# Optimization experiments

Measured on AMD Instinct MI355X. Metric: run time of the kernel, lower is better.

Reference implementation:

```python
import jax, jax.numpy as jnp
import numpy as np

B, T, D, E, K, OUT = 512, 2048, 32, 64, 8, 1024  # batch, tokens, feat(=32 hardcoded), experts, top-k, expert out dim


def setup_inputs() -> dict:
    key = jax.random.key(0)
    k0, k1, k2, k3 = jax.random.split(key, 4)
    x = jax.random.normal(k0, (B, T, D), jnp.float32)
    gate_w = jax.random.normal(k1, (E, D), jnp.float32) / np.sqrt(D)
    gate_b = jnp.zeros((E,), jnp.float32)
    # stacked expert Linear(32*k -> OUT): weight [E, OUT, D*K], bias [E, OUT]
    expert_w = jax.random.normal(k2, (E, OUT, D * K), jnp.float32) / np.sqrt(D * K)
    expert_b = jnp.zeros((E, OUT), jnp.float32)
    # gumbel noise for multinomial-without-replacement sampling (Gumbel top-k trick)
    gumbel = jax.random.gumbel(k3, (B, E, T), jnp.float32)
    return {"x": x, "gate_w": gate_w, "gate_b": gate_b,
            "expert_w": expert_w, "expert_b": expert_b, "gumbel": gumbel}


def reference(x, gate_w, gate_b, expert_w, expert_b, gumbel):
    # gate logits [B,T,E]; softmax over TOKEN axis (dim=-2 in torch)
    logits = jnp.einsum('btd,ed->bte', x, gate_w) + gate_b
    logp = jax.nn.log_softmax(logits, axis=-2)          # [B,T,E]
    # g = probs transposed to [B,E,T]; multinomial(k, no replacement) == top-k of log p + Gumbel
    scores = jnp.transpose(logp, (0, 2, 1)) + gumbel    # [B,E,T]
    _, idx = jax.lax.top_k(scores, K)                   # [B,E,K] sampled token indices
    # gather k tokens per (batch, expert): [B,E,K,D]
    gathered = jnp.take_along_axis(x[:, None, :, :], idx[..., None], axis=2)
    inp = gathered.reshape(B, E, K * D)                 # token-major concat, matches torch reshape
    # grouped per-expert GEMM + bias -> [B,E,OUT]
    out = jnp.einsum('bef,eof->beo', inp, expert_w) + expert_b[None]
    return out
```

## Files before the change

kernel.cpp:

```cpp
#include <hip/hip_runtime.h>
#include <hip/hip_bf16.h>
#include <stdint.h>

#define Bb   512
#define Tt   2048
#define Dd   32
#define Ee   64
#define Kk   8
#define OUTn 1024

typedef __attribute__((ext_vector_type(4))) float f32x4;
typedef __attribute__((ext_vector_type(2))) float f32x2;
typedef __attribute__((ext_vector_type(8))) short short8;
typedef __attribute__((ext_vector_type(4))) unsigned int uint4v;

static __device__ __forceinline__ uint32_t f2bf(float f) {
  uint32_t u = __float_as_uint(f);
  return (u + 0x7FFFu + ((u >> 16) & 1u)) >> 16;
}
static __device__ __forceinline__ uint32_t umax32(uint32_t a, uint32_t b){ return a > b ? a : b; }
static __device__ __forceinline__ uint32_t umin32(uint32_t a, uint32_t b){ return a < b ? a : b; }

#define RT_STRIDE 130

__global__ __launch_bounds__(512) void kA_select(
    const float* __restrict__ x,
    const float* __restrict__ gate_w,
    const float* __restrict__ gumbel,
    uint16_t* __restrict__ inp)
{
  const int b    = blockIdx.x;
  const int tid  = threadIdx.x;
  const int wave = tid >> 6;
  const int lane = tid & 63;
  const int l15  = lane & 15;
  const int l4   = lane >> 4;

  __shared__ __attribute__((aligned(16))) float r_tile[Ee * RT_STRIDE];

  short8 gfrag[4];
  #pragma unroll
  for (int c = 0; c < 4; ++c) {
    const float* gp = gate_w + (size_t)(c * 16 + l15) * Dd + l4 * 8;
    f32x4 g0 = *(const f32x4*)(gp);
    f32x4 g1 = *(const f32x4*)(gp + 4);
    short8 v;
    v[0] = (short)f2bf(g0[0]); v[1] = (short)f2bf(g0[1]);
    v[2] = (short)f2bf(g0[2]); v[3] = (short)f2bf(g0[3]);
    v[4] = (short)f2bf(g1[0]); v[5] = (short)f2bf(g1[1]);
    v[6] = (short)f2bf(g1[2]); v[7] = (short)f2bf(g1[3]);
    gfrag[c] = v;
  }

  uint32_t s[6][8];
  #pragma unroll
  for (int sl = 0; sl < 6; ++sl)
    #pragma unroll
    for (int el = 0; el < 8; ++el) s[sl][el] = 0u;

  for (int st = 0; st < 16; ++st) {
    const int t0 = st * 128;

    f32x2 gvv[8];
    #pragma unroll
    for (int el = 0; el < 8; ++el) {
      const int e = wave * 8 + el;
      gvv[el] = *(const f32x2*)(gumbel + ((size_t)b * Ee + e) * Tt + t0 + lane * 2);
    }

    {
      const int tloc = wave * 16;
      const float* xp = x + ((size_t)b * Tt + t0 + tloc + l15) * Dd + l4 * 8;
      f32x4 x0 = *(const f32x4*)(xp);
      f32x4 x1 = *(const f32x4*)(xp + 4);
      short8 bfr;
      bfr[0] = (short)f2bf(x0[0]); bfr[1] = (short)f2bf(x0[1]);
      bfr[2] = (short)f2bf(x0[2]); bfr[3] = (short)f2bf(x0[3]);
      bfr[4] = (short)f2bf(x1[0]); bfr[5] = (short)f2bf(x1[1]);
      bfr[6] = (short)f2bf(x1[2]); bfr[7] = (short)f2bf(x1[3]);
      #pragma unroll
      for (int c = 0; c < 4; ++c) {
        f32x4 acc = {0.f, 0.f, 0.f, 0.f};
        acc = __builtin_amdgcn_mfma_f32_16x16x32_bf16(gfrag[c], bfr, acc, 0, 0, 0);
        #pragma unroll
        for (int reg = 0; reg < 4; ++reg)
          r_tile[(c * 16 + l4 * 4 + reg) * RT_STRIDE + tloc + l15] = acc[reg];
      }
    }
    __syncthreads();

    #pragma unroll
    for (int el = 0; el < 8; ++el) {
      const int e = wave * 8 + el;
      f32x2 lv = *(const f32x2*)&r_tile[e * RT_STRIDE + lane * 2];
      #pragma unroll
      for (int j = 0; j < 2; ++j) {
        float rr = lv[j] + gvv[el][j];
        uint32_t u = __float_as_uint(rr);
        u = (u & 0x80000000u) ? ~u : (u | 0x80000000u);
        uint32_t key = (u & 0xFFFFF800u) | (2047u - (uint32_t)(t0 + lane * 2 + j));
        uint32_t c = umax32(s[5][el], key);
        uint32_t d;
        d = s[4][el]; s[5][el] = umin32(d, c); c = umax32(d, c);
        d = s[3][el]; s[4][el] = umin32(d, c); c = umax32(d, c);
        d = s[2][el]; s[3][el] = umin32(d, c); c = umax32(d, c);
        d = s[1][el]; s[2][el] = umin32(d, c); c = umax32(d, c);
        d = s[0][el]; s[1][el] = umin32(d, c); s[0][el] = umax32(d, c);
      }
    }
    __syncthreads();
  }

  #pragma unroll
  for (int el = 0; el < 8; ++el) {
    const int e = wave * 8 + el;
    uint32_t myT = 0;
    #pragma unroll
    for (int rnd = 0; rnd < 16; ++rnd) {
      uint32_t cur = s[0][el];
      uint32_t mx = cur;
      #pragma unroll
      for (int off = 1; off < 64; off <<= 1)
        mx = umax32(mx, (uint32_t)__shfl_xor((int)mx, off));
      uint32_t tw = 2047u - (mx & 2047u);
      if (lane == rnd) myT = tw;
      if (cur == mx) {
        s[0][el] = s[1][el]; s[1][el] = s[2][el]; s[2][el] = s[3][el];
        s[3][el] = s[4][el]; s[4][el] = s[5][el]; s[5][el] = 0u;
      }
    }

    const bool alive = lane < 16;
    double sc = -1e300;
    if (alive) {
      const float* xr = x + ((size_t)b * Tt + myT) * Dd;
      const float* gr = gate_w + (size_t)e * Dd;
      double a = 0.0;
      #pragma unroll
      for (int d = 0; d < Dd; ++d) a += (double)xr[d] * (double)gr[d];
      sc = a + (double)gumbel[((size_t)b * Ee + e) * Tt + myT];
    }
    uint32_t ti = alive ? myT : 0xFFFFu;
    double v = sc;
    uint32_t ord[8];
    #pragma unroll
    for (int k = 0; k < 8; ++k) {
      double bv = v; uint32_t bt = ti;
      #pragma unroll
      for (int off = 1; off < 64; off <<= 1) {
        double   ov = __shfl_xor(bv, off);
        uint32_t ot = (uint32_t)__shfl_xor((int)bt, off);
        if (ov > bv || (ov == bv && ot < bt)) { bv = ov; bt = ot; }
      }
      ord[k] = bt;
      if (ti == bt) v = -1e300;
    }

    const int kk = lane >> 3, sub = lane & 7;
    uint32_t tk = ord[0];
    #pragma unroll
    for (int q = 1; q < 8; ++q) tk = (kk == q) ? ord[q] : tk;
    const float* xs = x + ((size_t)b * Tt + tk) * Dd + sub * 4;
    f32x4 xv = *(const f32x4*)xs;
    uint32_t p0 = f2bf(xv[0]) | (f2bf(xv[1]) << 16);
    uint32_t p1 = f2bf(xv[2]) | (f2bf(xv[3]) << 16);
    uint32_t* dst = (uint32_t*)inp + ((((size_t)b * Ee + e) * 256) + kk * 32 + sub * 4) / 2;
    dst[0] = p0; dst[1] = p1;
  }
}

__global__ __launch_bounds__(256) void kB_gemm(
    const uint16_t* __restrict__ inp,
    const float* __restrict__ expert_w,
    const float* __restrict__ expert_b,
    float* __restrict__ out)
{
  const int bid = blockIdx.x;
  const int xcd = bid & 7;
  const int idx = bid >> 3;
  const int e   = xcd * 8 + (idx >> 5);
  const int rem = idx & 31;
  const int mb  = rem >> 3;
  const int nb  = rem & 7;
  const int b0 = mb * 128;
  const int o0 = nb * 128;
  const int tid  = threadIdx.x;
  const int wave = tid >> 6;
  const int lane = tid & 63;
  const int l15 = lane & 15, l4 = lane >> 4;
  const int wm = (wave & 1) * 64;
  const int wn = (wave >> 1) * 64;

  __shared__ __attribute__((aligned(16))) uint32_t Al[128 * 32];
  __shared__ __attribute__((aligned(16))) uint32_t Wl[128 * 32];

  f32x4 acc[4][4];
  #pragma unroll
  for (int i = 0; i < 4; ++i)
    #pragma unroll
    for (int j = 0; j < 4; ++j) acc[i][j] = (f32x4){0.f, 0.f, 0.f, 0.f};

  for (int ks = 0; ks < 4; ++ks) {
    #pragma unroll
    for (int i = 0; i < 4; ++i) {
      int gi = tid + i * 256;
      int m = gi >> 3, q = gi & 7;
      const uint4v* src = (const uint4v*)(inp + ((size_t)(b0 + m) * Ee + e) * 256 + ks * 64 + q * 8);
      *(uint4v*)&Al[m * 32 + ((q ^ (m & 7)) * 4)] = *src;
    }
    #pragma unroll
    for (int i = 0; i < 4; ++i) {
      int gi = tid + i * 256;
      int o = gi >> 3, q = gi & 7;
      const float* src = expert_w + ((size_t)e * OUTn + o0 + o) * 256 + ks * 64 + q * 8;
      f32x4 w0 = *(const f32x4*)src;
      f32x4 w1 = *(const f32x4*)(src + 4);
      uint4v v;
      v[0] = f2bf(w0[0]) | (f2bf(w0[1]) << 16);
      v[1] = f2bf(w0[2]) | (f2bf(w0[3]) << 16);
      v[2] = f2bf(w1[0]) | (f2bf(w1[1]) << 16);
      v[3] = f2bf(w1[2]) | (f2bf(w1[3]) << 16);
      *(uint4v*)&Wl[o * 32 + ((q ^ (o & 7)) * 4)] = v;
    }
    __syncthreads();

    short8 af[4][2], bf[4][2];
    #pragma unroll
    for (int mf = 0; mf < 4; ++mf)
      #pragma unroll
      for (int kb = 0; kb < 2; ++kb) {
        int row = wm + mf * 16 + l15;
        int g = kb * 4 + l4;
        af[mf][kb] = *(const short8*)&Al[row * 32 + ((g ^ (row & 7)) * 4)];
      }
    #pragma unroll
    for (int nf = 0; nf < 4; ++nf)
      #pragma unroll
      for (int kb = 0; kb < 2; ++kb) {
        int row = wn + nf * 16 + l15;
        int g = kb * 4 + l4;
        bf[nf][kb] = *(const short8*)&Wl[row * 32 + ((g ^ (row & 7)) * 4)];
      }
    #pragma unroll
    for (int mf = 0; mf < 4; ++mf)
      #pragma unroll
      for (int nf = 0; nf < 4; ++nf)
        #pragma unroll
        for (int kb = 0; kb < 2; ++kb)
          acc[mf][nf] = __builtin_amdgcn_mfma_f32_16x16x32_bf16(af[mf][kb], bf[nf][kb], acc[mf][nf], 0, 0, 0);
    __syncthreads();
  }

  #pragma unroll
  for (int nf = 0; nf < 4; ++nf) {
    const int ocol = o0 + wn + nf * 16 + l15;
    const float bias = expert_b[(size_t)e * OUTn + ocol];
    #pragma unroll
    for (int mf = 0; mf < 4; ++mf) {
      #pragma unroll
      for (int reg = 0; reg < 4; ++reg) {
        const int mrow = b0 + wm + mf * 16 + l4 * 4 + reg;
        out[((size_t)mrow * Ee + e) * OUTn + ocol] = acc[mf][nf][reg] + bias;
      }
    }
  }
}

extern "C" void kernel_launch(void* const* d_in, const int* in_sizes, int n_in,
                              void* d_out, int out_size, void* d_ws, size_t ws_size,
                              hipStream_t stream) {
  const float* x        = (const float*)d_in[0];
  const float* gate_w   = (const float*)d_in[1];
  const float* expert_w = (const float*)d_in[3];
  const float* expert_b = (const float*)d_in[4];
  const float* gumbel   = (const float*)d_in[5];

  uint16_t* inp = (uint16_t*)d_ws;

  kA_select<<<Bb, 512, 0, stream>>>(x, gate_w, gumbel, inp);
  kB_gemm<<<2048, 256, 0, stream>>>(inp, expert_w, expert_b, (float*)d_out);
}
```

Before: 263.0 us.

## Keep MFMA logits in registers and software-pipeline gumbel/x loads in select kernel

```diff
diff --git a/kernel.cpp b/kernel.cpp
--- a/kernel.cpp
+++ b/kernel.cpp
@@ -10,7 +10,6 @@
 #define OUTn 1024
 
 typedef __attribute__((ext_vector_type(4))) float f32x4;
-typedef __attribute__((ext_vector_type(2))) float f32x2;
 typedef __attribute__((ext_vector_type(8))) short short8;
 typedef __attribute__((ext_vector_type(4))) unsigned int uint4v;
 
@@ -21,9 +20,7 @@
 static __device__ __forceinline__ uint32_t umax32(uint32_t a, uint32_t b){ return a > b ? a : b; }
 static __device__ __forceinline__ uint32_t umin32(uint32_t a, uint32_t b){ return a < b ? a : b; }
 
-#define RT_STRIDE 130
-
-__global__ __launch_bounds__(512) void kA_select(
+__global__ __launch_bounds__(512, 4) void kA_select(
     const float* __restrict__ x,
     const float* __restrict__ gate_w,
     const float* __restrict__ gumbel,
@@ -35,113 +32,127 @@
   const int lane = tid & 63;
   const int l15  = lane & 15;
   const int l4   = lane >> 4;
-
-  __shared__ __attribute__((aligned(16))) float r_tile[Ee * RT_STRIDE];
-
-  short8 gfrag[4];
-  #pragma unroll
-  for (int c = 0; c < 4; ++c) {
+  const int c    = wave & 3;
+  const int h    = wave >> 2;
+
+  __shared__ uint32_t cand[Ee][32];
+
+  short8 gfrag;
+  {
     const float* gp = gate_w + (size_t)(c * 16 + l15) * Dd + l4 * 8;
     f32x4 g0 = *(const f32x4*)(gp);
     f32x4 g1 = *(const f32x4*)(gp + 4);
-    short8 v;
-    v[0] = (short)f2bf(g0[0]); v[1] = (short)f2bf(g0[1]);
-    v[2] = (short)f2bf(g0[2]); v[3] = (short)f2bf(g0[3]);
-    v[4] = (short)f2bf(g1[0]); v[5] = (short)f2bf(g1[1]);
-    v[6] = (short)f2bf(g1[2]); v[7] = (short)f2bf(g1[3]);
-    gfrag[c] = v;
-  }
-
-  uint32_t s[6][8];
-  #pragma unroll
-  for (int sl = 0; sl < 6; ++sl)
-    #pragma unroll
-    for (int el = 0; el < 8; ++el) s[sl][el] = 0u;
-
-  for (int st = 0; st < 16; ++st) {
-    const int t0 = st * 128;
-
-    f32x2 gvv[8];
-    #pragma unroll
-    for (int el = 0; el < 8; ++el) {
-      const int e = wave * 8 + el;
-      gvv[el] = *(const f32x2*)(gumbel + ((size_t)b * Ee + e) * Tt + t0 + lane * 2);
-    }
-
-    {
-      const int tloc = wave * 16;
-      const float* xp = x + ((size_t)b * Tt + t0 + tloc + l15) * Dd + l4 * 8;
-      f32x4 x0 = *(const f32x4*)(xp);
-      f32x4 x1 = *(const f32x4*)(xp + 4);
+    gfrag[0] = (short)f2bf(g0[0]); gfrag[1] = (short)f2bf(g0[1]);
+    gfrag[2] = (short)f2bf(g0[2]); gfrag[3] = (short)f2bf(g0[3]);
+    gfrag[4] = (short)f2bf(g1[0]); gfrag[5] = (short)f2bf(g1[1]);
+    gfrag[6] = (short)f2bf(g1[2]); gfrag[7] = (short)f2bf(g1[3]);
+  }
+
+  uint32_t s[4][8];
+  #pragma unroll
+  for (int r = 0; r < 4; ++r)
+    #pragma unroll
+    for (int j = 0; j < 8; ++j) s[r][j] = 0u;
+
+  const float* gum_base = gumbel + ((size_t)b * Ee + c * 16 + l4 * 4) * Tt + h * 1024 + l15;
+  const float* x_base   = x + ((size_t)b * Tt + h * 1024 + l15) * Dd + l4 * 8;
+  const int    tbase    = h * 1024 + l15;
+
+  auto load_set = [&](float (&G)[8], f32x4 (&XV)[4], int ii) {
+    #pragma unroll
+    for (int ss = 0; ss < 2; ++ss) {
+      #pragma unroll
+      for (int r = 0; r < 4; ++r)
+        G[ss * 4 + r] = gum_base[(size_t)r * Tt + ii * 32 + ss * 16];
+      #pragma unroll
+      for (int hv = 0; hv < 2; ++hv)
+        XV[ss * 2 + hv] = *(const f32x4*)(x_base + (size_t)(ii * 32 + ss * 16) * Dd + hv * 4);
+    }
+  };
+
+  auto proc_set = [&](float (&G)[8], f32x4 (&XV)[4], int ii) {
+    #pragma unroll
+    for (int ss = 0; ss < 2; ++ss) {
+      f32x4 lo = XV[ss * 2], hi = XV[ss * 2 + 1];
       short8 bfr;
-      bfr[0] = (short)f2bf(x0[0]); bfr[1] = (short)f2bf(x0[1]);
-      bfr[2] = (short)f2bf(x0[2]); bfr[3] = (short)f2bf(x0[3]);
-      bfr[4] = (short)f2bf(x1[0]); bfr[5] = (short)f2bf(x1[1]);
-      bfr[6] = (short)f2bf(x1[2]); bfr[7] = (short)f2bf(x1[3]);
-      #pragma unroll
-      for (int c = 0; c < 4; ++c) {
-        f32x4 acc = {0.f, 0.f, 0.f, 0.f};
-        acc = __builtin_amdgcn_mfma_f32_16x16x32_bf16(gfrag[c], bfr, acc, 0, 0, 0);
-        #pragma unroll
-        for (int reg = 0; reg < 4; ++reg)
-          r_tile[(c * 16 + l4 * 4 + reg) * RT_STRIDE + tloc + l15] = acc[reg];
-      }
-    }
-    __syncthreads();
-
-    #pragma unroll
-    for (int el = 0; el < 8; ++el) {
-      const int e = wave * 8 + el;
-      f32x2 lv = *(const f32x2*)&r_tile[e * RT_STRIDE + lane * 2];
-      #pragma unroll
-      for (int j = 0; j < 2; ++j) {
-        float rr = lv[j] + gvv[el][j];
-        uint32_t u = __float_as_uint(rr);
+      bfr[0] = (short)f2bf(lo[0]); bfr[1] = (short)f2bf(lo[1]);
+      bfr[2] = (short)f2bf(lo[2]); bfr[3] = (short)f2bf(lo[3]);
+      bfr[4] = (short)f2bf(hi[0]); bfr[5] = (short)f2bf(hi[1]);
+      bfr[6] = (short)f2bf(hi[2]); bfr[7] = (short)f2bf(hi[3]);
+      f32x4 acc = {0.f, 0.f, 0.f, 0.f};
+      acc = __builtin_amdgcn_mfma_f32_16x16x32_bf16(gfrag, bfr, acc, 0, 0, 0);
+      const uint32_t tl = 2047u - (uint32_t)(tbase + ii * 32 + ss * 16);
+      #pragma unroll
+      for (int r = 0; r < 4; ++r) {
+        float sc = acc[r] + G[ss * 4 + r];
+        uint32_t u = __float_as_uint(sc);
         u = (u & 0x80000000u) ? ~u : (u | 0x80000000u);
-        uint32_t key = (u & 0xFFFFF800u) | (2047u - (uint32_t)(t0 + lane * 2 + j));
-        uint32_t c = umax32(s[5][el], key);
-        uint32_t d;
-        d = s[4][el]; s[5][el] = umin32(d, c); c = umax32(d, c);
-        d = s[3][el]; s[4][el] = umin32(d, c); c = umax32(d, c);
-        d = s[2][el]; s[3][el] = umin32(d, c); c = umax32(d, c);
-        d = s[1][el]; s[2][el] = umin32(d, c); c = umax32(d, c);
-        d = s[0][el]; s[1][el] = umin32(d, c); s[0][el] = umax32(d, c);
-      }
-    }
-    __syncthreads();
-  }
-
-  #pragma unroll
+        uint32_t key = (u & 0xFFFFF800u) | tl;
+        uint32_t cc = umax32(s[r][7], key);
+        uint32_t dd;
+        dd = s[r][6]; s[r][7] = umin32(dd, cc); cc = umax32(dd, cc);
+        dd = s[r][5]; s[r][6] = umin32(dd, cc); cc = umax32(dd, cc);
+        dd = s[r][4]; s[r][5] = umin32(dd, cc); cc = umax32(dd, cc);
+        dd = s[r][3]; s[r][4] = umin32(dd, cc); cc = umax32(dd, cc);
+        dd = s[r][2]; s[r][3] = umin32(dd, cc); cc = umax32(dd, cc);
+        dd = s[r][1]; s[r][2] = umin32(dd, cc); cc = umax32(dd, cc);
+        dd = s[r][0]; s[r][1] = umin32(dd, cc); s[r][0] = umax32(dd, cc);
+      }
+    }
+  };
+
+  float gA[8]; f32x4 xA[4];
+  float gB[8]; f32x4 xB[4];
+  load_set(gA, xA, 0);
+  for (int i = 0; i < 32; i += 2) {
+    load_set(gB, xB, i + 1);
+    proc_set(gA, xA, i);
+    load_set(gA, xA, (i + 2 < 32) ? (i + 2) : 0);
+    proc_set(gB, xB, i + 1);
+  }
+
+  #pragma unroll
+  for (int r = 0; r < 4; ++r) {
+    const int e_abs = c * 16 + l4 * 4 + r;
+    #pragma unroll
+    for (int rnd = 0; rnd < 16; ++rnd) {
+      uint32_t cur = s[r][0];
+      uint32_t mx = cur;
+      mx = umax32(mx, (uint32_t)__shfl_xor((int)mx, 1));
+      mx = umax32(mx, (uint32_t)__shfl_xor((int)mx, 2));
+      mx = umax32(mx, (uint32_t)__shfl_xor((int)mx, 4));
+      mx = umax32(mx, (uint32_t)__shfl_xor((int)mx, 8));
+      if (l15 == rnd) cand[e_abs][h * 16 + rnd] = mx;
+      const bool pop = (cur == mx);
+      s[r][0] = pop ? s[r][1] : s[r][0];
+      s[r][1] = pop ? s[r][2] : s[r][1];
+      s[r][2] = pop ? s[r][3] : s[r][2];
+      s[r][3] = pop ? s[r][4] : s[r][3];
+      s[r][4] = pop ? s[r][5] : s[r][4];
+      s[r][5] = pop ? s[r][6] : s[r][5];
+      s[r][6] = pop ? s[r][7] : s[r][6];
+      s[r][7] = pop ? 0u      : s[r][7];
+    }
+  }
+  __syncthreads();
+
+  #pragma unroll 1
   for (int el = 0; el < 8; ++el) {
     const int e = wave * 8 + el;
-    uint32_t myT = 0;
-    #pragma unroll
-    for (int rnd = 0; rnd < 16; ++rnd) {
-      uint32_t cur = s[0][el];
-      uint32_t mx = cur;
-      #pragma unroll
-      for (int off = 1; off < 64; off <<= 1)
-        mx = umax32(mx, (uint32_t)__shfl_xor((int)mx, off));
-      uint32_t tw = 2047u - (mx & 2047u);
-      if (lane == rnd) myT = tw;
-      if (cur == mx) {
-        s[0][el] = s[1][el]; s[1][el] = s[2][el]; s[2][el] = s[3][el];
-        s[3][el] = s[4][el]; s[4][el] = s[5][el]; s[5][el] = 0u;
-      }
-    }
-
-    const bool alive = lane < 16;
-    double sc = -1e300;
+    const bool alive = lane < 32;
+    uint32_t myT = 2047;
+    double v = -1e300;
     if (alive) {
+      uint32_t key = cand[e][lane];
+      myT = 2047u - (key & 2047u);
       const float* xr = x + ((size_t)b * Tt + myT) * Dd;
       const float* gr = gate_w + (size_t)e * Dd;
       double a = 0.0;
       #pragma unroll
       for (int d = 0; d < Dd; ++d) a += (double)xr[d] * (double)gr[d];
-      sc = a + (double)gumbel[((size_t)b * Ee + e) * Tt + myT];
+      v = a + (double)gumbel[((size_t)b * Ee + e) * Tt + myT];
     }
     uint32_t ti = alive ? myT : 0xFFFFu;
-    double v = sc;
     uint32_t ord[8];
     #pragma unroll
     for (int k = 0; k < 8; ++k) {
```

New measurement: 246.3 us. 6.3% less time.
